# Optimization experiments

Hardware: AMD Instinct MI355X
Metric: run time of the kernel (lower is better)

Reference implementation:

```python
import jax, jax.numpy as jnp
import numpy as np

B, M, K, C = 256, 512, 6, 32  # graphs, nodes/graph, knn k, channels
IN_DIM, OUT_DIM = 4, 6


def setup_inputs() -> dict:
    key = jax.random.key(0)
    ks = jax.random.split(key, 20)
    N = B * M
    x = jax.random.normal(ks[0], (N, 1), dtype=jnp.float32)
    pos = jax.random.uniform(ks[1], (N, 3), dtype=jnp.float32)
    batch = jnp.repeat(jnp.arange(B, dtype=jnp.int64), M)

    def lin(k, out_d, in_d):
        bound = 1.0 / np.sqrt(in_d)
        kw, kb = jax.random.split(k)
        W = jax.random.uniform(kw, (out_d, in_d), minval=-bound, maxval=bound, dtype=jnp.float32)
        b = jax.random.uniform(kb, (out_d,), minval=-bound, maxval=bound, dtype=jnp.float32)
        return W, b

    W1a, b1a = lin(ks[2], C, IN_DIM)
    W2a, b2a = lin(ks[3], C, C)
    W1b, b1b = lin(ks[4], C, C)
    W2b, b2b = lin(ks[5], C, C)
    W1c, b1c = lin(ks[6], C, C)
    W2c, b2c = lin(ks[7], C, C)
    Wr, br = lin(ks[8], OUT_DIM, C)
    return dict(x=x, pos=pos, batch=batch,
                W1a=W1a, b1a=b1a, W2a=W2a, b2a=b2a,
                W1b=W1b, b1b=b1b, W2b=W2b, b2b=b2b,
                W1c=W1c, b1c=b1c, W2c=W2c, b2c=b2c,
                Wr=Wr, br=br)


def knn_indices(pos3):
    # pos3: [B, M, 3] -> [B, M, K] indices of K nearest neighbors (self included, loop=True)
    sq = jnp.sum(pos3 * pos3, axis=-1)                      # [B, M]
    d2 = sq[:, :, None] + sq[:, None, :] - 2.0 * jnp.einsum('bmd,bnd->bmn', pos3, pos3)
    _, idx = jax.lax.top_k(-d2, K)                          # [B, M, K]
    return idx


def gcn_layer(h, idx, W1, b1, W2, b2):
    # h: [B, M, Cin]; gather h_j per edge, 2-layer MLP per edge, max-aggregate over neighbors
    Cin = h.shape[-1]
    nb = jnp.take_along_axis(h, idx.reshape(B, M * K, 1), axis=1).reshape(B, M, K, Cin)
    msg = jax.nn.relu(jnp.einsum('bmkc,oc->bmko', nb, W1) + b1)
    msg = jnp.einsum('bmkc,oc->bmko', msg, W2) + b2
    return jnp.max(msg, axis=2)                             # max aggregation -> [B, M, C]


def reference(x, pos, batch,
              W1a, b1a, W2a, b2a,
              W1b, b1b, W2b, b2b,
              W1c, b1c, W2c, b2c,
              Wr, br):
    pos3 = pos.reshape(B, M, 3)
    idx = knn_indices(pos3)
    h = jnp.concatenate([x, pos], axis=-1).reshape(B, M, IN_DIM)
    h = jax.nn.relu(gcn_layer(h, idx, W1a, b1a, W2a, b2a))
    h = jax.nn.relu(gcn_layer(h, idx, W1b, b1b, W2b, b2b))
    h = jax.nn.relu(gcn_layer(h, idx, W1c, b1c, W2c, b2c))
    g = jnp.max(h, axis=1)                                  # global_max_pool -> [B, C]
    return g @ Wr.T + br                                    # [B, 6]
```

## Files before the change

kernel.cpp:

```cpp
#include <hip/hip_runtime.h>
#include <cstddef>
#include <cstdint>

#define NB 256
#define M 512
#define KNN 6
#define C 32

__global__ __launch_bounds__(1024, 1) void megafused_kernel(
    const float* __restrict__ x, const float* __restrict__ pos,
    const float* __restrict__ W1a, const float* __restrict__ b1a,
    const float* __restrict__ W2a, const float* __restrict__ b2a,
    const float* __restrict__ W1b, const float* __restrict__ b1b,
    const float* __restrict__ W2b, const float* __restrict__ b2b,
    const float* __restrict__ W1c, const float* __restrict__ b1c,
    const float* __restrict__ W2c, const float* __restrict__ b2c,
    const float* __restrict__ Wr,  const float* __restrict__ br,
    float* __restrict__ out)
{
    __shared__ __align__(16) float Ts[M * C];
    const int g  = blockIdx.x;
    const int t  = threadIdx.x;
    const int n  = t & (M - 1);
    const int hv = t >> 9;
    const int c0 = __builtin_amdgcn_readfirstlane(hv << 4);

    float4* sp    = (float4*)Ts;
    float4* lists = (float4*)(Ts + 2048);

    const float* p = pos + (size_t)g * M * 3;
    if (t < M) {
        float xx = p[3*t], yy = p[3*t+1], zz = p[3*t+2];
        sp[t] = make_float4(xx, yy, zz, fmaf(xx, xx, fmaf(yy, yy, zz * zz)));
    }
    __syncthreads();

    const float4 pm = sp[n];

    float d0 = INFINITY, d1 = INFINITY, d2 = INFINITY,
          d3 = INFINITY, d4 = INFINITY, d5 = INFINITY;
    int   i0 = -1, i1 = -1, i2 = -1, i3 = -1, i4 = -1, i5 = -1;

    const int col0 = hv << 8;
#pragma unroll 8
    for (int jj = 0; jj < 256; jj++) {
        const int col = col0 + jj;
        const float4 pn = sp[col];
        float dot  = fmaf(pm.x, pn.x, fmaf(pm.y, pn.y, pm.z * pn.z));
        float dist = fmaf(-2.f, dot, pm.w + pn.w);
        bool c5 = dist < d5, c4 = dist < d4, c3 = dist < d3,
             c2 = dist < d2, c1 = dist < d1, cz = dist < d0;
        i5 = c4 ? i4 : (c5 ? col : i5);
        i4 = c3 ? i3 : (c4 ? col : i4);
        i3 = c2 ? i2 : (c3 ? col : i3);
        i2 = c1 ? i1 : (c2 ? col : i2);
        i1 = cz ? i0 : (c1 ? col : i1);
        i0 = cz ? col : i0;
        d5 = __builtin_amdgcn_fmed3f(dist, d4, d5);
        d4 = __builtin_amdgcn_fmed3f(dist, d3, d4);
        d3 = __builtin_amdgcn_fmed3f(dist, d2, d3);
        d2 = __builtin_amdgcn_fmed3f(dist, d1, d2);
        d1 = __builtin_amdgcn_fmed3f(dist, d0, d1);
        d0 = fminf(dist, d0);
    }

    {
        unsigned pa = (unsigned)i0 | ((unsigned)i1 << 10) | ((unsigned)i2 << 20);
        unsigned pb = (unsigned)i3 | ((unsigned)i4 << 10) | ((unsigned)i5 << 20);
        lists[2*t]     = make_float4(d0, d1, d2, d3);
        lists[2*t + 1] = make_float4(d4, d5, __uint_as_float(pa), __uint_as_float(pb));
    }
    __syncthreads();

    int j[KNN];
    {
        const int pt = t ^ M;
        const float4 q0 = lists[2*pt], q1 = lists[2*pt + 1];
        const unsigned ppa = __float_as_uint(q1.z), ppb = __float_as_uint(q1.w);

        float md[KNN]; int mi[KNN]; float sd[KNN]; int si[KNN];
        if (c0 == 0) {
            md[0]=d0; md[1]=d1; md[2]=d2; md[3]=d3; md[4]=d4; md[5]=d5;
            mi[0]=i0; mi[1]=i1; mi[2]=i2; mi[3]=i3; mi[4]=i4; mi[5]=i5;
            sd[0]=q0.x; sd[1]=q0.y; sd[2]=q0.z; sd[3]=q0.w; sd[4]=q1.x; sd[5]=q1.y;
            si[0]=(int)(ppa & 1023); si[1]=(int)((ppa >> 10) & 1023); si[2]=(int)((ppa >> 20) & 1023);
            si[3]=(int)(ppb & 1023); si[4]=(int)((ppb >> 10) & 1023); si[5]=(int)((ppb >> 20) & 1023);
        } else {
            md[0]=q0.x; md[1]=q0.y; md[2]=q0.z; md[3]=q0.w; md[4]=q1.x; md[5]=q1.y;
            mi[0]=(int)(ppa & 1023); mi[1]=(int)((ppa >> 10) & 1023); mi[2]=(int)((ppa >> 20) & 1023);
            mi[3]=(int)(ppb & 1023); mi[4]=(int)((ppb >> 10) & 1023); mi[5]=(int)((ppb >> 20) & 1023);
            sd[0]=d0; sd[1]=d1; sd[2]=d2; sd[3]=d3; sd[4]=d4; sd[5]=d5;
            si[0]=i0; si[1]=i1; si[2]=i2; si[3]=i3; si[4]=i4; si[5]=i5;
        }
#pragma unroll
        for (int k = 0; k < KNN; k++) {
            const float dist = sd[k];
            const int   nn   = si[k];
            bool c5m = dist < md[5], c4m = dist < md[4], c3m = dist < md[3],
                 c2m = dist < md[2], c1m = dist < md[1], czm = dist < md[0];
            mi[5] = c4m ? mi[4] : (c5m ? nn : mi[5]);
            mi[4] = c3m ? mi[3] : (c4m ? nn : mi[4]);
            mi[3] = c2m ? mi[2] : (c3m ? nn : mi[3]);
            mi[2] = c1m ? mi[1] : (c2m ? nn : mi[2]);
            mi[1] = czm ? mi[0] : (c1m ? nn : mi[1]);
            mi[0] = czm ? nn : mi[0];
            md[5] = __builtin_amdgcn_fmed3f(dist, md[4], md[5]);
            md[4] = __builtin_amdgcn_fmed3f(dist, md[3], md[4]);
            md[3] = __builtin_amdgcn_fmed3f(dist, md[2], md[3]);
            md[2] = __builtin_amdgcn_fmed3f(dist, md[1], md[2]);
            md[1] = __builtin_amdgcn_fmed3f(dist, md[0], md[1]);
            md[0] = fminf(dist, md[0]);
        }
#pragma unroll
        for (int k = 0; k < KNN; k++) j[k] = mi[k];
    }
    __syncthreads();

    const int ne     = n & 3;
    const int nb_own = (n << 7) + ((hv ^ ((n >> 2) & 1)) << 6);
    const int nb_par = nb_own ^ 64;
    char* TsB = (char*)Ts;

    int jb[KNN], je[KNN];
#pragma unroll
    for (int k = 0; k < KNN; k++) {
        const int jl = j[k];
        jb[k] = (jl << 7) + ((hv ^ ((jl >> 2) & 1)) << 6);
        je[k] = jl & 3;
    }

    {
        const float h0 = x[(size_t)g * M + n];
        const float h1 = pm.x, h2 = pm.y, h3 = pm.z;
        float m1[C];
#pragma unroll
        for (int o = 0; o < C; o++) {
            float a = b1a[o];
            a = fmaf(W1a[o*4+0], h0, a);
            a = fmaf(W1a[o*4+1], h1, a);
            a = fmaf(W1a[o*4+2], h2, a);
            a = fmaf(W1a[o*4+3], h3, a);
            m1[o] = fmaxf(a, 0.f);
        }
#pragma unroll
        for (int q2 = 0; q2 < 4; q2++) {
            float4 v; float* vp = &v.x;
#pragma unroll
            for (int u = 0; u < 4; u++) {
                const int o = c0 + q2*4 + u;
                float a = b2a[o];
#pragma unroll
                for (int i = 0; i < C; i++) a = fmaf(W2a[o*C + i], m1[i], a);
                vp[u] = a;
            }
            *(float4*)(TsB + nb_own + ((q2 ^ ne) << 4)) = v;
        }
    }
    __syncthreads();

#pragma unroll 1
    for (int layer = 0; layer < 2; layer++) {
        const float* W1 = layer ? W1c : W1b;
        const float* b1 = layer ? b1c : b1b;
        const float* W2 = layer ? W2c : W2b;
        const float* b2 = layer ? b2c : b2b;

        float hm[16];
#pragma unroll
        for (int u = 0; u < 16; u++) hm[u] = 0.f;
#pragma unroll
        for (int k = 0; k < KNN; k++) {
#pragma unroll
            for (int q2 = 0; q2 < 4; q2++) {
                const float4 v = *(const float4*)(TsB + jb[k] + ((q2 ^ je[k]) << 4));
                hm[4*q2+0] = fmaxf(hm[4*q2+0], v.x);
                hm[4*q2+1] = fmaxf(hm[4*q2+1], v.y);
                hm[4*q2+2] = fmaxf(hm[4*q2+2], v.z);
                hm[4*q2+3] = fmaxf(hm[4*q2+3], v.w);
            }
        }
        __syncthreads();
#pragma unroll
        for (int q2 = 0; q2 < 4; q2++)
            *(float4*)(TsB + nb_own + ((q2 ^ ne) << 4)) =
                make_float4(hm[4*q2+0], hm[4*q2+1], hm[4*q2+2], hm[4*q2+3]);
        __syncthreads();
        float hf[C];
        if (c0 == 0) {
#pragma unroll
            for (int u = 0; u < 16; u++) hf[u] = hm[u];
#pragma unroll
            for (int q2 = 0; q2 < 4; q2++) {
                const float4 v = *(const float4*)(TsB + nb_par + ((q2 ^ ne) << 4));
                hf[16+4*q2+0]=v.x; hf[16+4*q2+1]=v.y; hf[16+4*q2+2]=v.z; hf[16+4*q2+3]=v.w;
            }
        } else {
#pragma unroll
            for (int u = 0; u < 16; u++) hf[16+u] = hm[u];
#pragma unroll
            for (int q2 = 0; q2 < 4; q2++) {
                const float4 v = *(const float4*)(TsB + nb_par + ((q2 ^ ne) << 4));
                hf[4*q2+0]=v.x; hf[4*q2+1]=v.y; hf[4*q2+2]=v.z; hf[4*q2+3]=v.w;
            }
        }
        __syncthreads();
        float m1h[16];
#pragma unroll
        for (int o2 = 0; o2 < 16; o2++) {
            const int o = c0 + o2;
            float a = b1[o];
#pragma unroll
            for (int i = 0; i < C; i++) a = fmaf(W1[o*C + i], hf[i], a);
            m1h[o2] = fmaxf(a, 0.f);
        }
#pragma unroll
        for (int q2 = 0; q2 < 4; q2++)
            *(float4*)(TsB + nb_own + ((q2 ^ ne) << 4)) =
                make_float4(m1h[4*q2+0], m1h[4*q2+1], m1h[4*q2+2], m1h[4*q2+3]);
        __syncthreads();
        float m1f[C];
        if (c0 == 0) {
#pragma unroll
            for (int u = 0; u < 16; u++) m1f[u] = m1h[u];
#pragma unroll
            for (int q2 = 0; q2 < 4; q2++) {
                const float4 v = *(const float4*)(TsB + nb_par + ((q2 ^ ne) << 4));
                m1f[16+4*q2+0]=v.x; m1f[16+4*q2+1]=v.y; m1f[16+4*q2+2]=v.z; m1f[16+4*q2+3]=v.w;
            }
        } else {
#pragma unroll
            for (int u = 0; u < 16; u++) m1f[16+u] = m1h[u];
#pragma unroll
            for (int q2 = 0; q2 < 4; q2++) {
                const float4 v = *(const float4*)(TsB + nb_par + ((q2 ^ ne) << 4));
                m1f[4*q2+0]=v.x; m1f[4*q2+1]=v.y; m1f[4*q2+2]=v.z; m1f[4*q2+3]=v.w;
            }
        }
        __syncthreads();
#pragma unroll
        for (int q2 = 0; q2 < 4; q2++) {
            float4 v; float* vp = &v.x;
#pragma unroll
            for (int u = 0; u < 4; u++) {
                const int o = c0 + q2*4 + u;
                float a = b2[o];
#pragma unroll
                for (int i = 0; i < C; i++) a = fmaf(W2[o*C + i], m1f[i], a);
                vp[u] = a;
            }
            *(float4*)(TsB + nb_own + ((q2 ^ ne) << 4)) = v;
        }
        __syncthreads();
    }

    {
        const int c   = t & 31;
        const int grp = t >> 5;
        float m = 0.f;
#pragma unroll
        for (int r16 = 0; r16 < 16; r16++) {
            const int r = (grp << 4) + r16;
            m = fmaxf(m, Ts[(r << 5) + ((((c >> 2) ^ (r & 7)) << 2) | (c & 3))]);
        }
        __syncthreads();
        Ts[(grp << 5) + (c ^ grp)] = m;
        __syncthreads();
        if (t < 32) {
            float mm = 0.f;
#pragma unroll
            for (int g2 = 0; g2 < 32; g2++)
                mm = fmaxf(mm, Ts[(g2 << 5) + (t ^ g2)]);
            Ts[t] = mm;
        }
        __syncthreads();
    }

    if (t < 6) {
        float a = br[t];
#pragma unroll
        for (int i = 0; i < C; i++) a = fmaf(Wr[t*C + i], Ts[i], a);
        out[g * 6 + t] = a;
    }
}

extern "C" void kernel_launch(void* const* d_in, const int* in_sizes, int n_in,
                              void* d_out, int out_size, void* d_ws, size_t ws_size,
                              hipStream_t stream) {
    const float* x   = (const float*)d_in[0];
    const float* pos = (const float*)d_in[1];
    const float* W1a = (const float*)d_in[3];
    const float* b1a = (const float*)d_in[4];
    const float* W2a = (const float*)d_in[5];
    const float* b2a = (const float*)d_in[6];
    const float* W1b = (const float*)d_in[7];
    const float* b1b = (const float*)d_in[8];
    const float* W2b = (const float*)d_in[9];
    const float* b2b = (const float*)d_in[10];
    const float* W1c = (const float*)d_in[11];
    const float* b1c = (const float*)d_in[12];
    const float* W2c = (const float*)d_in[13];
    const float* b2c = (const float*)d_in[14];
    const float* Wr  = (const float*)d_in[15];
    const float* br  = (const float*)d_in[16];

    float* out = (float*)d_out;

    megafused_kernel<<<NB, 1024, 0, stream>>>(x, pos,
                                              W1a, b1a, W2a, b2a,
                                              W1b, b1b, W2b, b2b,
                                              W1c, b1c, W2c, b2c,
                                              Wr, br, out);
}
```

Measured before the change: 172.9 us.

## Use one thread per node instead of two-thread split per node

The block shrinks from 1024 to 512 threads, so each thread handles one node end to end. It scans all 512 candidates for its kNN list and computes all 32 channels of each MLP layer. This removes the partner top-k merge, the shared-memory exchange of half-channel vectors and several block barriers per layer. In exchange there are half as many waves per CU to hide LDS and VALU latency, and each thread's serial kNN loop is twice as long.

```diff
diff --git a/kernel.cpp b/kernel.cpp
--- a/kernel.cpp
+++ b/kernel.cpp
@@ -7,7 +7,7 @@
 #define KNN 6
 #define C 32
 
-__global__ __launch_bounds__(1024, 1) void megafused_kernel(
+__global__ __launch_bounds__(512, 1) void megafused_kernel(
     const float* __restrict__ x, const float* __restrict__ pos,
     const float* __restrict__ W1a, const float* __restrict__ b1a,
     const float* __restrict__ W2a, const float* __restrict__ b2a,
@@ -19,32 +19,27 @@
     float* __restrict__ out)
 {
     __shared__ __align__(16) float Ts[M * C];
-    const int g  = blockIdx.x;
-    const int t  = threadIdx.x;
-    const int n  = t & (M - 1);
-    const int hv = t >> 9;
-    const int c0 = __builtin_amdgcn_readfirstlane(hv << 4);
-
-    float4* sp    = (float4*)Ts;
-    float4* lists = (float4*)(Ts + 2048);
+    const int g = blockIdx.x;
+    const int t = threadIdx.x;
+    const int n = t;
+
+    float4* sp = (float4*)Ts;
 
     const float* p = pos + (size_t)g * M * 3;
-    if (t < M) {
-        float xx = p[3*t], yy = p[3*t+1], zz = p[3*t+2];
-        sp[t] = make_float4(xx, yy, zz, fmaf(xx, xx, fmaf(yy, yy, zz * zz)));
-    }
+    const float xx = p[3*t], yy = p[3*t+1], zz = p[3*t+2];
+    const float h0 = x[(size_t)g * M + n];
+    const float pw = fmaf(xx, xx, fmaf(yy, yy, zz * zz));
+    sp[t] = make_float4(xx, yy, zz, pw);
     __syncthreads();
 
-    const float4 pm = sp[n];
+    const float4 pm = make_float4(xx, yy, zz, pw);
 
     float d0 = INFINITY, d1 = INFINITY, d2 = INFINITY,
           d3 = INFINITY, d4 = INFINITY, d5 = INFINITY;
     int   i0 = -1, i1 = -1, i2 = -1, i3 = -1, i4 = -1, i5 = -1;
 
-    const int col0 = hv << 8;
 #pragma unroll 8
-    for (int jj = 0; jj < 256; jj++) {
-        const int col = col0 + jj;
+    for (int col = 0; col < M; col++) {
         const float4 pn = sp[col];
         float dot  = fmaf(pm.x, pn.x, fmaf(pm.y, pn.y, pm.z * pn.z));
         float dist = fmaf(-2.f, dot, pm.w + pn.w);
@@ -63,74 +58,18 @@
         d1 = __builtin_amdgcn_fmed3f(dist, d0, d1);
         d0 = fminf(dist, d0);
     }
-
+    __syncthreads();
+
+    const int np = n & 7;
+    char* TsB = (char*)Ts;
+    int jb[KNN], jp[KNN];
     {
-        unsigned pa = (unsigned)i0 | ((unsigned)i1 << 10) | ((unsigned)i2 << 20);
-        unsigned pb = (unsigned)i3 | ((unsigned)i4 << 10) | ((unsigned)i5 << 20);
-        lists[2*t]     = make_float4(d0, d1, d2, d3);
-        lists[2*t + 1] = make_float4(d4, d5, __uint_as_float(pa), __uint_as_float(pb));
-    }
-    __syncthreads();
-
-    int j[KNN];
+        int j0=i0, j1=i1, j2=i2, j3=i3, j4=i4, j5=i5;
+        jb[0]=j0<<7; jb[1]=j1<<7; jb[2]=j2<<7; jb[3]=j3<<7; jb[4]=j4<<7; jb[5]=j5<<7;
+        jp[0]=j0&7;  jp[1]=j1&7;  jp[2]=j2&7;  jp[3]=j3&7;  jp[4]=j4&7;  jp[5]=j5&7;
+    }
+
     {
-        const int pt = t ^ M;
-        const float4 q0 = lists[2*pt], q1 = lists[2*pt + 1];
-        const unsigned ppa = __float_as_uint(q1.z), ppb = __float_as_uint(q1.w);
-
-        float md[KNN]; int mi[KNN]; float sd[KNN]; int si[KNN];
-        if (c0 == 0) {
-            md[0]=d0; md[1]=d1; md[2]=d2; md[3]=d3; md[4]=d4; md[5]=d5;
-            mi[0]=i0; mi[1]=i1; mi[2]=i2; mi[3]=i3; mi[4]=i4; mi[5]=i5;
-            sd[0]=q0.x; sd[1]=q0.y; sd[2]=q0.z; sd[3]=q0.w; sd[4]=q1.x; sd[5]=q1.y;
-            si[0]=(int)(ppa & 1023); si[1]=(int)((ppa >> 10) & 1023); si[2]=(int)((ppa >> 20) & 1023);
-            si[3]=(int)(ppb & 1023); si[4]=(int)((ppb >> 10) & 1023); si[5]=(int)((ppb >> 20) & 1023);
-        } else {
-            md[0]=q0.x; md[1]=q0.y; md[2]=q0.z; md[3]=q0.w; md[4]=q1.x; md[5]=q1.y;
-            mi[0]=(int)(ppa & 1023); mi[1]=(int)((ppa >> 10) & 1023); mi[2]=(int)((ppa >> 20) & 1023);
-            mi[3]=(int)(ppb & 1023); mi[4]=(int)((ppb >> 10) & 1023); mi[5]=(int)((ppb >> 20) & 1023);
-            sd[0]=d0; sd[1]=d1; sd[2]=d2; sd[3]=d3; sd[4]=d4; sd[5]=d5;
-            si[0]=i0; si[1]=i1; si[2]=i2; si[3]=i3; si[4]=i4; si[5]=i5;
-        }
-#pragma unroll
-        for (int k = 0; k < KNN; k++) {
-            const float dist = sd[k];
-            const int   nn   = si[k];
-            bool c5m = dist < md[5], c4m = dist < md[4], c3m = dist < md[3],
-                 c2m = dist < md[2], c1m = dist < md[1], czm = dist < md[0];
-            mi[5] = c4m ? mi[4] : (c5m ? nn : mi[5]);
-            mi[4] = c3m ? mi[3] : (c4m ? nn : mi[4]);
-            mi[3] = c2m ? mi[2] : (c3m ? nn : mi[3]);
-            mi[2] = c1m ? mi[1] : (c2m ? nn : mi[2]);
-            mi[1] = czm ? mi[0] : (c1m ? nn : mi[1]);
-            mi[0] = czm ? nn : mi[0];
-            md[5] = __builtin_amdgcn_fmed3f(dist, md[4], md[5]);
-            md[4] = __builtin_amdgcn_fmed3f(dist, md[3], md[4]);
-            md[3] = __builtin_amdgcn_fmed3f(dist, md[2], md[3]);
-            md[2] = __builtin_amdgcn_fmed3f(dist, md[1], md[2]);
-            md[1] = __builtin_amdgcn_fmed3f(dist, md[0], md[1]);
-            md[0] = fminf(dist, md[0]);
-        }
-#pragma unroll
-        for (int k = 0; k < KNN; k++) j[k] = mi[k];
-    }
-    __syncthreads();
-
-    const int ne     = n & 3;
-    const int nb_own = (n << 7) + ((hv ^ ((n >> 2) & 1)) << 6);
-    const int nb_par = nb_own ^ 64;
-    char* TsB = (char*)Ts;
-
-    int jb[KNN], je[KNN];
-#pragma unroll
-    for (int k = 0; k < KNN; k++) {
-        const int jl = j[k];
-        jb[k] = (jl << 7) + ((hv ^ ((jl >> 2) & 1)) << 6);
-        je[k] = jl & 3;
-    }
-
-    {
-        const float h0 = x[(size_t)g * M + n];
         const float h1 = pm.x, h2 = pm.y, h3 = pm.z;
         float m1[C];
 #pragma unroll
@@ -143,17 +82,17 @@
             m1[o] = fmaxf(a, 0.f);
         }
 #pragma unroll
-        for (int q2 = 0; q2 < 4; q2++) {
+        for (int q = 0; q < 8; q++) {
             float4 v; float* vp = &v.x;
 #pragma unroll
             for (int u = 0; u < 4; u++) {
-                const int o = c0 + q2*4 + u;
+                const int o = 4*q + u;
                 float a = b2a[o];
 #pragma unroll
                 for (int i = 0; i < C; i++) a = fmaf(W2a[o*C + i], m1[i], a);
                 vp[u] = a;
             }
-            *(float4*)(TsB + nb_own + ((q2 ^ ne) << 4)) = v;
+            *(float4*)(TsB + (n << 7) + ((q ^ np) << 4)) = v;
         }
     }
     __syncthreads();
@@ -165,90 +104,42 @@
         const float* W2 = layer ? W2c : W2b;
         const float* b2 = layer ? b2c : b2b;
 
-        float hm[16];
-#pragma unroll
-        for (int u = 0; u < 16; u++) hm[u] = 0.f;
+        float hm[C];
+#pragma unroll
+        for (int u = 0; u < C; u++) hm[u] = 0.f;
 #pragma unroll
         for (int k = 0; k < KNN; k++) {
 #pragma unroll
-            for (int q2 = 0; q2 < 4; q2++) {
-                const float4 v = *(const float4*)(TsB + jb[k] + ((q2 ^ je[k]) << 4));
-                hm[4*q2+0] = fmaxf(hm[4*q2+0], v.x);
-                hm[4*q2+1] = fmaxf(hm[4*q2+1], v.y);
-                hm[4*q2+2] = fmaxf(hm[4*q2+2], v.z);
-                hm[4*q2+3] = fmaxf(hm[4*q2+3], v.w);
+            for (int q = 0; q < 8; q++) {
+                const float4 v = *(const float4*)(TsB + jb[k] + ((q ^ jp[k]) << 4));
+                hm[4*q+0] = fmaxf(hm[4*q+0], v.x);
+                hm[4*q+1] = fmaxf(hm[4*q+1], v.y);
+                hm[4*q+2] = fmaxf(hm[4*q+2], v.z);
+                hm[4*q+3] = fmaxf(hm[4*q+3], v.w);
             }
         }
         __syncthreads();
-#pragma unroll
-        for (int q2 = 0; q2 < 4; q2++)
-            *(float4*)(TsB + nb_own + ((q2 ^ ne) << 4)) =
-                make_float4(hm[4*q2+0], hm[4*q2+1], hm[4*q2+2], hm[4*q2+3]);
-        __syncthreads();
-        float hf[C];
-        if (c0 == 0) {
-#pragma unroll
-            for (int u = 0; u < 16; u++) hf[u] = hm[u];
-#pragma unroll
-            for (int q2 = 0; q2 < 4; q2++) {
-                const float4 v = *(const float4*)(TsB + nb_par + ((q2 ^ ne) << 4));
-                hf[16+4*q2+0]=v.x; hf[16+4*q2+1]=v.y; hf[16+4*q2+2]=v.z; hf[16+4*q2+3]=v.w;
-            }
-        } else {
-#pragma unroll
-            for (int u = 0; u < 16; u++) hf[16+u] = hm[u];
-#pragma unroll
-            for (int q2 = 0; q2 < 4; q2++) {
-                const float4 v = *(const float4*)(TsB + nb_par + ((q2 ^ ne) << 4));
-                hf[4*q2+0]=v.x; hf[4*q2+1]=v.y; hf[4*q2+2]=v.z; hf[4*q2+3]=v.w;
-            }
-        }
-        __syncthreads();
-        float m1h[16];
-#pragma unroll
-        for (int o2 = 0; o2 < 16; o2++) {
-            const int o = c0 + o2;
+
+        float m1[C];
+#pragma unroll
+        for (int o = 0; o < C; o++) {
             float a = b1[o];
 #pragma unroll
-            for (int i = 0; i < C; i++) a = fmaf(W1[o*C + i], hf[i], a);
-            m1h[o2] = fmaxf(a, 0.f);
-        }
-#pragma unroll
-        for (int q2 = 0; q2 < 4; q2++)
-            *(float4*)(TsB + nb_own + ((q2 ^ ne) << 4)) =
-                make_float4(m1h[4*q2+0], m1h[4*q2+1], m1h[4*q2+2], m1h[4*q2+3]);
-        __syncthreads();
-        float m1f[C];
-        if (c0 == 0) {
-#pragma unroll
-            for (int u = 0; u < 16; u++) m1f[u] = m1h[u];
-#pragma unroll
-            for (int q2 = 0; q2 < 4; q2++) {
-                const float4 v = *(const float4*)(TsB + nb_par + ((q2 ^ ne) << 4));
-                m1f[16+4*q2+0]=v.x; m1f[16+4*q2+1]=v.y; m1f[16+4*q2+2]=v.z; m1f[16+4*q2+3]=v.w;
-            }
-        } else {
-#pragma unroll
-            for (int u = 0; u < 16; u++) m1f[16+u] = m1h[u];
-#pragma unroll
-            for (int q2 = 0; q2 < 4; q2++) {
-                const float4 v = *(const float4*)(TsB + nb_par + ((q2 ^ ne) << 4));
-                m1f[4*q2+0]=v.x; m1f[4*q2+1]=v.y; m1f[4*q2+2]=v.z; m1f[4*q2+3]=v.w;
-            }
-        }
-        __syncthreads();
-#pragma unroll
-        for (int q2 = 0; q2 < 4; q2++) {
+            for (int i = 0; i < C; i++) a = fmaf(W1[o*C + i], hm[i], a);
+            m1[o] = fmaxf(a, 0.f);
+        }
+#pragma unroll
+        for (int q = 0; q < 8; q++) {
             float4 v; float* vp = &v.x;
 #pragma unroll
             for (int u = 0; u < 4; u++) {
-                const int o = c0 + q2*4 + u;
+                const int o = 4*q + u;
                 float a = b2[o];
 #pragma unroll
-                for (int i = 0; i < C; i++) a = fmaf(W2[o*C + i], m1f[i], a);
+                for (int i = 0; i < C; i++) a = fmaf(W2[o*C + i], m1[i], a);
                 vp[u] = a;
             }
-            *(float4*)(TsB + nb_own + ((q2 ^ ne) << 4)) = v;
+            *(float4*)(TsB + (n << 7) + ((q ^ np) << 4)) = v;
         }
         __syncthreads();
     }
@@ -258,8 +149,8 @@
         const int grp = t >> 5;
         float m = 0.f;
 #pragma unroll
-        for (int r16 = 0; r16 < 16; r16++) {
-            const int r = (grp << 4) + r16;
+        for (int r32 = 0; r32 < 32; r32++) {
+            const int r = (grp << 5) + r32;
             m = fmaxf(m, Ts[(r << 5) + ((((c >> 2) ^ (r & 7)) << 2) | (c & 3))]);
         }
         __syncthreads();
@@ -268,18 +159,16 @@
         if (t < 32) {
             float mm = 0.f;
 #pragma unroll
-            for (int g2 = 0; g2 < 32; g2++)
+            for (int g2 = 0; g2 < 16; g2++)
                 mm = fmaxf(mm, Ts[(g2 << 5) + (t ^ g2)]);
             Ts[t] = mm;
         }
-        __syncthreads();
-    }
-
-    if (t < 6) {
-        float a = br[t];
-#pragma unroll
-        for (int i = 0; i < C; i++) a = fmaf(Wr[t*C + i], Ts[i], a);
-        out[g * 6 + t] = a;
+        if (t < 6) {
+            float a = br[t];
+#pragma unroll
+            for (int i = 0; i < C; i++) a = fmaf(Wr[t*C + i], Ts[i], a);
+            out[g * 6 + t] = a;
+        }
     }
 }
 
@@ -305,9 +194,9 @@
 
     float* out = (float*)d_out;
 
-    megafused_kernel<<<NB, 1024, 0, stream>>>(x, pos,
-                                              W1a, b1a, W2a, b2a,
-                                              W1b, b1b, W2b, b2b,
-                                              W1c, b1c, W2c, b2c,
-                                              Wr, br, out);
+    megafused_kernel<<<NB, 512, 0, stream>>>(x, pos,
+                                             W1a, b1a, W2a, b2a,
+                                             W1b, b1b, W2b, b2b,
+                                             W1c, b1c, W2c, b2c,
+                                             Wr, br, out);
 }
```

After: 203.7 us. 1.18x slower.

## Gather all channels per thread and compute first MLP layer redundantly

Applied to the files above, without the earlier changes.

In the two inner GCN layers, each thread now gathers all 32 channels of its neighbours and computes the full 32x32 first MLP layer itself. Before, each half of the block handled 16 channels and the halves swapped partial results through shared memory. This drops four block-wide barriers and two LDS exchange rounds per layer. The cost is twice the LDS gather traffic, twice the W1 FMAs per thread, and more live registers (hm[32], m1[32]). Under the 1024-thread launch bound that register growth risks spilling.

```diff
diff --git a/kernel.cpp b/kernel.cpp
--- a/kernel.cpp
+++ b/kernel.cpp
@@ -33,6 +33,7 @@
         float xx = p[3*t], yy = p[3*t+1], zz = p[3*t+2];
         sp[t] = make_float4(xx, yy, zz, fmaf(xx, xx, fmaf(yy, yy, zz * zz)));
     }
+    const float h0 = x[(size_t)g * M + n];
     __syncthreads();
 
     const float4 pm = sp[n];
@@ -118,19 +119,16 @@
 
     const int ne     = n & 3;
     const int nb_own = (n << 7) + ((hv ^ ((n >> 2) & 1)) << 6);
-    const int nb_par = nb_own ^ 64;
     char* TsB = (char*)Ts;
 
-    int jb[KNN], je[KNN];
+    int jb[KNN], jp_[KNN];
 #pragma unroll
     for (int k = 0; k < KNN; k++) {
-        const int jl = j[k];
-        jb[k] = (jl << 7) + ((hv ^ ((jl >> 2) & 1)) << 6);
-        je[k] = jl & 3;
-    }
-
-    {
-        const float h0 = x[(size_t)g * M + n];
+        jb[k]  = j[k] << 7;
+        jp_[k] = j[k] & 7;
+    }
+
+    {
         const float h1 = pm.x, h2 = pm.y, h3 = pm.z;
         float m1[C];
 #pragma unroll
@@ -165,78 +163,30 @@
         const float* W2 = layer ? W2c : W2b;
         const float* b2 = layer ? b2c : b2b;
 
-        float hm[16];
-#pragma unroll
-        for (int u = 0; u < 16; u++) hm[u] = 0.f;
+        float hm[C];
+#pragma unroll
+        for (int u = 0; u < C; u++) hm[u] = 0.f;
 #pragma unroll
         for (int k = 0; k < KNN; k++) {
 #pragma unroll
-            for (int q2 = 0; q2 < 4; q2++) {
-                const float4 v = *(const float4*)(TsB + jb[k] + ((q2 ^ je[k]) << 4));
-                hm[4*q2+0] = fmaxf(hm[4*q2+0], v.x);
-                hm[4*q2+1] = fmaxf(hm[4*q2+1], v.y);
-                hm[4*q2+2] = fmaxf(hm[4*q2+2], v.z);
-                hm[4*q2+3] = fmaxf(hm[4*q2+3], v.w);
+            for (int q = 0; q < 8; q++) {
+                const float4 v = *(const float4*)(TsB + jb[k] + ((q ^ jp_[k]) << 4));
+                hm[4*q+0] = fmaxf(hm[4*q+0], v.x);
+                hm[4*q+1] = fmaxf(hm[4*q+1], v.y);
+                hm[4*q+2] = fmaxf(hm[4*q+2], v.z);
+                hm[4*q+3] = fmaxf(hm[4*q+3], v.w);
             }
         }
         __syncthreads();
-#pragma unroll
-        for (int q2 = 0; q2 < 4; q2++)
-            *(float4*)(TsB + nb_own + ((q2 ^ ne) << 4)) =
-                make_float4(hm[4*q2+0], hm[4*q2+1], hm[4*q2+2], hm[4*q2+3]);
-        __syncthreads();
-        float hf[C];
-        if (c0 == 0) {
-#pragma unroll
-            for (int u = 0; u < 16; u++) hf[u] = hm[u];
-#pragma unroll
-            for (int q2 = 0; q2 < 4; q2++) {
-                const float4 v = *(const float4*)(TsB + nb_par + ((q2 ^ ne) << 4));
-                hf[16+4*q2+0]=v.x; hf[16+4*q2+1]=v.y; hf[16+4*q2+2]=v.z; hf[16+4*q2+3]=v.w;
-            }
-        } else {
-#pragma unroll
-            for (int u = 0; u < 16; u++) hf[16+u] = hm[u];
-#pragma unroll
-            for (int q2 = 0; q2 < 4; q2++) {
-                const float4 v = *(const float4*)(TsB + nb_par + ((q2 ^ ne) << 4));
-                hf[4*q2+0]=v.x; hf[4*q2+1]=v.y; hf[4*q2+2]=v.z; hf[4*q2+3]=v.w;
-            }
-        }
-        __syncthreads();
-        float m1h[16];
-#pragma unroll
-        for (int o2 = 0; o2 < 16; o2++) {
-            const int o = c0 + o2;
+
+        float m1[C];
+#pragma unroll
+        for (int o = 0; o < C; o++) {
             float a = b1[o];
 #pragma unroll
-            for (int i = 0; i < C; i++) a = fmaf(W1[o*C + i], hf[i], a);
-            m1h[o2] = fmaxf(a, 0.f);
-        }
-#pragma unroll
-        for (int q2 = 0; q2 < 4; q2++)
-            *(float4*)(TsB + nb_own + ((q2 ^ ne) << 4)) =
-                make_float4(m1h[4*q2+0], m1h[4*q2+1], m1h[4*q2+2], m1h[4*q2+3]);
-        __syncthreads();
-        float m1f[C];
-        if (c0 == 0) {
-#pragma unroll
-            for (int u = 0; u < 16; u++) m1f[u] = m1h[u];
-#pragma unroll
-            for (int q2 = 0; q2 < 4; q2++) {
-                const float4 v = *(const float4*)(TsB + nb_par + ((q2 ^ ne) << 4));
-                m1f[16+4*q2+0]=v.x; m1f[16+4*q2+1]=v.y; m1f[16+4*q2+2]=v.z; m1f[16+4*q2+3]=v.w;
-            }
-        } else {
-#pragma unroll
-            for (int u = 0; u < 16; u++) m1f[16+u] = m1h[u];
-#pragma unroll
-            for (int q2 = 0; q2 < 4; q2++) {
-                const float4 v = *(const float4*)(TsB + nb_par + ((q2 ^ ne) << 4));
-                m1f[4*q2+0]=v.x; m1f[4*q2+1]=v.y; m1f[4*q2+2]=v.z; m1f[4*q2+3]=v.w;
-            }
-        }
-        __syncthreads();
+            for (int i = 0; i < C; i++) a = fmaf(W1[o*C + i], hm[i], a);
+            m1[o] = fmaxf(a, 0.f);
+        }
 #pragma unroll
         for (int q2 = 0; q2 < 4; q2++) {
             float4 v; float* vp = &v.x;
@@ -245,7 +195,7 @@
                 const int o = c0 + q2*4 + u;
                 float a = b2[o];
 #pragma unroll
-                for (int i = 0; i < C; i++) a = fmaf(W2[o*C + i], m1f[i], a);
+                for (int i = 0; i < C; i++) a = fmaf(W2[o*C + i], m1[i], a);
                 vp[u] = a;
             }
             *(float4*)(TsB + nb_own + ((q2 ^ ne) << 4)) = v;
```

After: 195.3 us. 1.13x slower.

## Double-buffer LDS to drop barriers and precompute position table in pre-kernel

Applied to the files above, without the earlier changes.

Splits the single shared buffer into two ping-pong buffers so that reads and writes of consecutive stages land in different buffers, which lets several __syncthreads be removed. A separate prepass kernel builds a global float4 (x,y,z,|p|^2) table, and the kNN loop reads neighbours from global/L1 instead of LDS. This avoids the initial barrier but adds a kernel launch, and the hot kNN loop now depends on cache hits. LDS use doubles to 128KB per block, which may constrain occupancy or fail to fit.

```diff
diff --git a/kernel.cpp b/kernel.cpp
--- a/kernel.cpp
+++ b/kernel.cpp
@@ -7,8 +7,19 @@
 #define KNN 6
 #define C 32
 
+
+__global__ __launch_bounds__(512, 1) void build_table_kernel(
+    const float* __restrict__ pos, float4* __restrict__ tab)
+{
+    const int i = blockIdx.x * 512 + threadIdx.x;
+    const float xx = pos[3*i], yy = pos[3*i+1], zz = pos[3*i+2];
+    tab[i] = make_float4(xx, yy, zz, fmaf(xx, xx, fmaf(yy, yy, zz * zz)));
+}
+
+template <bool USE_TAB>
 __global__ __launch_bounds__(1024, 1) void megafused_kernel(
     const float* __restrict__ x, const float* __restrict__ pos,
+    const float4* __restrict__ tab,
     const float* __restrict__ W1a, const float* __restrict__ b1a,
     const float* __restrict__ W2a, const float* __restrict__ b2a,
     const float* __restrict__ W1b, const float* __restrict__ b1b,
@@ -18,34 +29,41 @@
     const float* __restrict__ Wr,  const float* __restrict__ br,
     float* __restrict__ out)
 {
-    __shared__ __align__(16) float Ts[M * C];
+    __shared__ __align__(16) float Pbuf[M * C];
+    __shared__ __align__(16) float Qbuf[M * C];
     const int g  = blockIdx.x;
     const int t  = threadIdx.x;
     const int n  = t & (M - 1);
     const int hv = t >> 9;
     const int c0 = __builtin_amdgcn_readfirstlane(hv << 4);
 
-    float4* sp    = (float4*)Ts;
-    float4* lists = (float4*)(Ts + 2048);
-
-    const float* p = pos + (size_t)g * M * 3;
-    if (t < M) {
-        float xx = p[3*t], yy = p[3*t+1], zz = p[3*t+2];
-        sp[t] = make_float4(xx, yy, zz, fmaf(xx, xx, fmaf(yy, yy, zz * zz)));
-    }
-    __syncthreads();
-
-    const float4 pm = sp[n];
+    float4* sp    = (float4*)Qbuf;
+    float4* lists = (float4*)(Qbuf + 2048);
+
+    const float4* tabg = tab + (size_t)g * M;
+    float4 pm;
+    if constexpr (USE_TAB) {
+        pm = tabg[n];
+    } else {
+        const float* p = pos + (size_t)g * M * 3;
+        if (t < M) {
+            float xx = p[3*t], yy = p[3*t+1], zz = p[3*t+2];
+            sp[t] = make_float4(xx, yy, zz, fmaf(xx, xx, fmaf(yy, yy, zz * zz)));
+        }
+    }
+    const float h0 = x[(size_t)g * M + n];
+    if constexpr (!USE_TAB) { __syncthreads(); pm = sp[n]; }
 
     float d0 = INFINITY, d1 = INFINITY, d2 = INFINITY,
           d3 = INFINITY, d4 = INFINITY, d5 = INFINITY;
     int   i0 = -1, i1 = -1, i2 = -1, i3 = -1, i4 = -1, i5 = -1;
 
-    const int col0 = hv << 8;
 #pragma unroll 8
     for (int jj = 0; jj < 256; jj++) {
-        const int col = col0 + jj;
-        const float4 pn = sp[col];
+        const int col = (c0 << 4) + jj;
+        float4 pn;
+        if constexpr (USE_TAB) pn = tabg[col];
+        else                   pn = sp[col];
         float dot  = fmaf(pm.x, pn.x, fmaf(pm.y, pn.y, pm.z * pn.z));
         float dist = fmaf(-2.f, dot, pm.w + pn.w);
         bool c5 = dist < d5, c4 = dist < d4, c3 = dist < d3,
@@ -114,12 +132,10 @@
 #pragma unroll
         for (int k = 0; k < KNN; k++) j[k] = mi[k];
     }
-    __syncthreads();
 
     const int ne     = n & 3;
     const int nb_own = (n << 7) + ((hv ^ ((n >> 2) & 1)) << 6);
     const int nb_par = nb_own ^ 64;
-    char* TsB = (char*)Ts;
 
     int jb[KNN], je[KNN];
 #pragma unroll
@@ -130,7 +146,6 @@
     }
 
     {
-        const float h0 = x[(size_t)g * M + n];
         const float h1 = pm.x, h2 = pm.y, h3 = pm.z;
         float m1[C];
 #pragma unroll
@@ -153,7 +168,7 @@
                 for (int i = 0; i < C; i++) a = fmaf(W2a[o*C + i], m1[i], a);
                 vp[u] = a;
             }
-            *(float4*)(TsB + nb_own + ((q2 ^ ne) << 4)) = v;
+            *(float4*)((char*)Pbuf + nb_own + ((q2 ^ ne) << 4)) = v;
         }
     }
     __syncthreads();
@@ -164,6 +179,8 @@
         const float* b1 = layer ? b1c : b1b;
         const float* W2 = layer ? W2c : W2b;
         const float* b2 = layer ? b2c : b2b;
+        char* src = (char*)(layer ? Qbuf : Pbuf);
+        char* dst = (char*)(layer ? Pbuf : Qbuf);
 
         float hm[16];
 #pragma unroll
@@ -172,17 +189,16 @@
         for (int k = 0; k < KNN; k++) {
 #pragma unroll
             for (int q2 = 0; q2 < 4; q2++) {
-                const float4 v = *(const float4*)(TsB + jb[k] + ((q2 ^ je[k]) << 4));
+                const float4 v = *(const float4*)(src + jb[k] + ((q2 ^ je[k]) << 4));
                 hm[4*q2+0] = fmaxf(hm[4*q2+0], v.x);
                 hm[4*q2+1] = fmaxf(hm[4*q2+1], v.y);
                 hm[4*q2+2] = fmaxf(hm[4*q2+2], v.z);
                 hm[4*q2+3] = fmaxf(hm[4*q2+3], v.w);
             }
         }
-        __syncthreads();
 #pragma unroll
         for (int q2 = 0; q2 < 4; q2++)
-            *(float4*)(TsB + nb_own + ((q2 ^ ne) << 4)) =
+            *(float4*)(dst + nb_own + ((q2 ^ ne) << 4)) =
                 make_float4(hm[4*q2+0], hm[4*q2+1], hm[4*q2+2], hm[4*q2+3]);
         __syncthreads();
         float hf[C];
@@ -191,7 +207,7 @@
             for (int u = 0; u < 16; u++) hf[u] = hm[u];
 #pragma unroll
             for (int q2 = 0; q2 < 4; q2++) {
-                const float4 v = *(const float4*)(TsB + nb_par + ((q2 ^ ne) << 4));
+                const float4 v = *(const float4*)(dst + nb_par + ((q2 ^ ne) << 4));
                 hf[16+4*q2+0]=v.x; hf[16+4*q2+1]=v.y; hf[16+4*q2+2]=v.z; hf[16+4*q2+3]=v.w;
             }
         } else {
@@ -199,11 +215,10 @@
             for (int u = 0; u < 16; u++) hf[16+u] = hm[u];
 #pragma unroll
             for (int q2 = 0; q2 < 4; q2++) {
-                const float4 v = *(const float4*)(TsB + nb_par + ((q2 ^ ne) << 4));
+                const float4 v = *(const float4*)(dst + nb_par + ((q2 ^ ne) << 4));
                 hf[4*q2+0]=v.x; hf[4*q2+1]=v.y; hf[4*q2+2]=v.z; hf[4*q2+3]=v.w;
             }
         }
-        __syncthreads();
         float m1h[16];
 #pragma unroll
         for (int o2 = 0; o2 < 16; o2++) {
@@ -215,7 +230,7 @@
         }
 #pragma unroll
         for (int q2 = 0; q2 < 4; q2++)
-            *(float4*)(TsB + nb_own + ((q2 ^ ne) << 4)) =
+            *(float4*)(src + nb_own + ((q2 ^ ne) << 4)) =
                 make_float4(m1h[4*q2+0], m1h[4*q2+1], m1h[4*q2+2], m1h[4*q2+3]);
         __syncthreads();
         float m1f[C];
@@ -224,7 +239,7 @@
             for (int u = 0; u < 16; u++) m1f[u] = m1h[u];
 #pragma unroll
             for (int q2 = 0; q2 < 4; q2++) {
-                const float4 v = *(const float4*)(TsB + nb_par + ((q2 ^ ne) << 4));
+                const float4 v = *(const float4*)(src + nb_par + ((q2 ^ ne) << 4));
                 m1f[16+4*q2+0]=v.x; m1f[16+4*q2+1]=v.y; m1f[16+4*q2+2]=v.z; m1f[16+4*q2+3]=v.w;
             }
         } else {
@@ -232,11 +247,10 @@
             for (int u = 0; u < 16; u++) m1f[16+u] = m1h[u];
 #pragma unroll
             for (int q2 = 0; q2 < 4; q2++) {
-                const float4 v = *(const float4*)(TsB + nb_par + ((q2 ^ ne) << 4));
+                const float4 v = *(const float4*)(src + nb_par + ((q2 ^ ne) << 4));
                 m1f[4*q2+0]=v.x; m1f[4*q2+1]=v.y; m1f[4*q2+2]=v.z; m1f[4*q2+3]=v.w;
             }
         }
-        __syncthreads();
 #pragma unroll
         for (int q2 = 0; q2 < 4; q2++) {
             float4 v; float* vp = &v.x;
@@ -248,7 +262,7 @@
                 for (int i = 0; i < C; i++) a = fmaf(W2[o*C + i], m1f[i], a);
                 vp[u] = a;
             }
-            *(float4*)(TsB + nb_own + ((q2 ^ ne) << 4)) = v;
+            *(float4*)(dst + nb_own + ((q2 ^ ne) << 4)) = v;
         }
         __syncthreads();
     }
@@ -260,17 +274,16 @@
 #pragma unroll
         for (int r16 = 0; r16 < 16; r16++) {
             const int r = (grp << 4) + r16;
-            m = fmaxf(m, Ts[(r << 5) + ((((c >> 2) ^ (r & 7)) << 2) | (c & 3))]);
-        }
-        __syncthreads();
-        Ts[(grp << 5) + (c ^ grp)] = m;
+            m = fmaxf(m, Pbuf[(r << 5) + ((((c >> 2) ^ (r & 7)) << 2) | (c & 3))]);
+        }
+        Qbuf[(grp << 5) + (c ^ grp)] = m;
         __syncthreads();
         if (t < 32) {
             float mm = 0.f;
 #pragma unroll
             for (int g2 = 0; g2 < 32; g2++)
-                mm = fmaxf(mm, Ts[(g2 << 5) + (t ^ g2)]);
-            Ts[t] = mm;
+                mm = fmaxf(mm, Qbuf[(g2 << 5) + (t ^ g2)]);
+            Qbuf[t] = mm;
         }
         __syncthreads();
     }
@@ -278,7 +291,7 @@
     if (t < 6) {
         float a = br[t];
 #pragma unroll
-        for (int i = 0; i < C; i++) a = fmaf(Wr[t*C + i], Ts[i], a);
+        for (int i = 0; i < C; i++) a = fmaf(Wr[t*C + i], Qbuf[i], a);
         out[g * 6 + t] = a;
     }
 }
@@ -304,10 +317,22 @@
     const float* br  = (const float*)d_in[16];
 
     float* out = (float*)d_out;
-
-    megafused_kernel<<<NB, 1024, 0, stream>>>(x, pos,
-                                              W1a, b1a, W2a, b2a,
-                                              W1b, b1b, W2b, b2b,
-                                              W1c, b1c, W2c, b2c,
-                                              Wr, br, out);
+    float4* tab = (float4*)d_ws;
+    const bool use_tab = (d_ws != nullptr) &&
+                         (ws_size >= sizeof(float4) * (size_t)NB * M);
+
+    if (use_tab) {
+        build_table_kernel<<<NB, 512, 0, stream>>>(pos, tab);
+        megafused_kernel<true><<<NB, 1024, 0, stream>>>(x, pos, tab,
+                                                        W1a, b1a, W2a, b2a,
+                                                        W1b, b1b, W2b, b2b,
+                                                        W1c, b1c, W2c, b2c,
+                                                        Wr, br, out);
+    } else {
+        megafused_kernel<false><<<NB, 1024, 0, stream>>>(x, pos, tab,
+                                                         W1a, b1a, W2a, b2a,
+                                                         W1b, b1b, W2b, b2b,
+                                                         W1c, b1c, W2c, b2c,
+                                                         Wr, br, out);
+    }
 }
```

Result: no change. 174.9 us (+1.2%).
